# Kernel optimization log

Measured on AMD Instinct MI355X. Metric: run time of the kernel, lower is better.

The kernel has to match this reference:

```python
import jax, jax.numpy as jnp
import numpy as np

EPS = 1e-12

def _l2norm(v):
    return v / (jnp.linalg.norm(v) + EPS)

def _spectral_norm_weight(W, u):
    # torch spectral_norm with n_power_iterations=1: v = norm(W^T u); u' = norm(W v);
    # sigma = u'^T W v with u', v detached; returns W / sigma.
    v = jax.lax.stop_gradient(_l2norm(W.T @ u))
    u2 = jax.lax.stop_gradient(_l2norm(W @ v))
    sigma = u2 @ (W @ v)
    return W / sigma

def setup_inputs() -> dict:
    key = jax.random.key(0)
    ks = jax.random.split(key, 8)
    C, H, W = 64, 96, 96
    Cfg = C // 8
    g = 1e-2  # small weight scale (module uses orthogonal init with tiny gain)
    return {
        "x":  jax.random.normal(ks[0], (1, C, H, W), jnp.float32),
        "Wf": jax.random.normal(ks[1], (Cfg, C), jnp.float32) * g,
        "bf": jnp.zeros((Cfg,), jnp.float32),
        "Wg": jax.random.normal(ks[2], (Cfg, C), jnp.float32) * g,
        "bg": jnp.zeros((Cfg,), jnp.float32),
        "Wh": jax.random.normal(ks[3], (C, C), jnp.float32) * g,
        "bh": jnp.zeros((C,), jnp.float32),
        "gamma": jax.random.normal(ks[4], (1,), jnp.float32),
        "uf": jax.random.normal(ks[5], (Cfg,), jnp.float32),
        "ug": jax.random.normal(ks[6], (Cfg,), jnp.float32),
        "uh": jax.random.normal(ks[7], (C,), jnp.float32),
    }

def reference(x, Wf, bf, Wg, bg, Wh, bh, gamma, uf, ug, uh):
    B, C, H, Wd = x.shape
    N = H * Wd
    xf = x.reshape(B, C, N)  # 1x1 convs act per-pixel -> matmul over channel dim
    Wf_sn = _spectral_norm_weight(Wf, uf)
    Wg_sn = _spectral_norm_weight(Wg, ug)
    Wh_sn = _spectral_norm_weight(Wh, uh)
    f_flat = jnp.einsum('oc,bcn->bon', Wf_sn, xf) + bf[:, None]  # [B,Cfg,N]
    g_flat = jnp.einsum('oc,bcn->bon', Wg_sn, xf) + bg[:, None]  # [B,Cfg,N]
    h_flat = jnp.einsum('oc,bcn->bon', Wh_sn, xf) + bh[:, None]  # [B,C,N]
    # s[b,n,m] = sum_k g[b,k,n] * f[b,k,m]  (g^T f)
    s = jnp.einsum('bkn,bkm->bnm', g_flat, f_flat)  # [B,N,N]
    beta = jax.nn.softmax(s, axis=1)                # softmax over dim=1 (g axis)
    o = jnp.einsum('bcn,bnm->bcm', h_flat, beta)    # [B,C,N]
    o = o.reshape(B, C, H, Wd)
    return gamma * o + x
```

## Files before the change

kernel.cpp:

```cpp
#include <hip/hip_runtime.h>
#include <hip/hip_bf16.h>

#define NPIX 9216
#define MTILES (NPIX / 16)

typedef __attribute__((ext_vector_type(4))) float f32x4;
typedef __attribute__((ext_vector_type(16))) float f32x16;
typedef __attribute__((ext_vector_type(8))) short bf16x8;
typedef __attribute__((ext_vector_type(2))) unsigned int u32x2;

__device__ __forceinline__ void gload_lds16(const void* g, void* l) {
  __builtin_amdgcn_global_load_lds(
      (const __attribute__((address_space(1))) unsigned int*)g,
      (__attribute__((address_space(3))) unsigned int*)l, 16, 0, 0);
}
__device__ __forceinline__ void gload_lds4(const void* g, void* l) {
  __builtin_amdgcn_global_load_lds(
      (const __attribute__((address_space(1))) unsigned int*)g,
      (__attribute__((address_space(3))) unsigned int*)l, 4, 0, 0);
}
#define LDS_OFF(p) ((unsigned)(unsigned long long)(const __attribute__((address_space(3))) char*)(const char*)(p))

__global__ __launch_bounds__(256) void fgh_kernel(
    const float* __restrict__ x,
    const float* __restrict__ Wf, const float* __restrict__ bfv,
    const float* __restrict__ Wg, const float* __restrict__ bgv,
    const float* __restrict__ Wh, const float* __restrict__ bhv,
    const float* __restrict__ uf, const float* __restrict__ ug,
    const float* __restrict__ uh,
    ushort* __restrict__ Qp, ushort* __restrict__ Kp, ushort* __restrict__ Vt2) {
  __shared__ float vsh3[3][64];
  __shared__ float is_s[3];
  const int tid = threadIdx.x;
  const int wv = tid >> 6, t = tid & 63;
  if (wv < 3) {
    const float* W = (wv == 0) ? Wf : (wv == 1) ? Wg : Wh;
    const float* u = (wv == 0) ? uf : (wv == 1) ? ug : uh;
    const int O = (wv == 2) ? 64 : 8;
    float v = 0.f;
    for (int o = 0; o < O; ++o) v += W[o * 64 + t] * u[o];
    float s = v * v;
    for (int off = 32; off; off >>= 1) s += __shfl_xor(s, off);
    vsh3[wv][t] = v / (sqrtf(s) + 1e-12f);
    float wvv = 0.f;
    if (t < O) { for (int c = 0; c < 64; ++c) wvv += W[t * 64 + c] * vsh3[wv][c]; }
    float s2 = (t < O) ? wvv * wvv : 0.f;
    for (int off = 32; off; off >>= 1) s2 += __shfl_xor(s2, off);
    const float nw = sqrtf(s2);
    if (t == 0) is_s[wv] = (nw + 1e-12f) / s2;
  }
  __syncthreads();

  const float LOG2E = 1.44269504f;
  const int px = tid & 63;
  const int rw = __builtin_amdgcn_readfirstlane(tid >> 6);
  const int r0 = blockIdx.y * 16 + rw * 4;
  const int p  = blockIdx.x * 64 + px;

  float xv[64];
  #pragma unroll
  for (int c = 0; c < 64; ++c) xv[c] = x[c * NPIX + p];

  const float* W0;
  float scl;
  if (r0 < 8)       { W0 = Wf + r0 * 64;        scl = is_s[0]; }
  else if (r0 < 16) { W0 = Wg + (r0 - 8) * 64;  scl = is_s[1]; }
  else              { W0 = Wh + (r0 - 16) * 64; scl = is_s[2]; }

  float acc[4] = {0.f, 0.f, 0.f, 0.f};
  #pragma unroll
  for (int c = 0; c < 64; ++c) {
    const float xc = xv[c];
    acc[0] += W0[c]       * xc;
    acc[1] += W0[64 + c]  * xc;
    acc[2] += W0[128 + c] * xc;
    acc[3] += W0[192 + c] * xc;
  }

  const int tile = p >> 5, nn = p & 31;
  const int kbase = tile * 512 + nn * 8;
  const int vfix = (nn >> 4) * 512 + ((nn >> 2) & 1) * 256
                 + (nn & 3) + 4 * ((nn >> 3) & 1);
  #pragma unroll
  for (int j = 0; j < 4; ++j) {
    const int r = r0 + j;
    if (r < 8) {
      const float val = (acc[j] * scl + bfv[r]) * LOG2E;
      const __hip_bfloat16 h = __float2bfloat16(val);
      Qp[p * 16 + r] = *(const ushort*)&h;
    } else if (r < 16) {
      const int rk = r - 8;
      const float val = acc[j] * scl + bgv[rk];
      const __hip_bfloat16 h = __float2bfloat16(val);
      Kp[kbase + rk] = *(const ushort*)&h;
    } else {
      const int rv = r - 16;
      const float val = acc[j] * scl + bhv[rv];
      const __hip_bfloat16 hv = __float2bfloat16(val);
      const int vidx = tile * 2048 + (rv >> 5) * 1024 + vfix + (rv & 31) * 8;
      Vt2[vidx] = *(const ushort*)&hv;
    }
  }
}

template <int S>
__global__ __launch_bounds__(256) void attn_kernel(
    const ushort* __restrict__ Qp, const ushort* __restrict__ Kp,
    const ushort* __restrict__ Vt2,
    ushort* __restrict__ Om,
    float* __restrict__ Sm) {
  constexpr int NSEG = NPIX / S;
  constexpr int NT = NSEG / 32;
  __shared__ ushort Vs[4][2048];
  __shared__ ushort Ks[4][512];
  const int tid  = threadIdx.x;
  const int w    = tid >> 6;
  const int l    = tid & 63;
  const int cc   = l & 31;
  const int h    = l >> 5;
  const int spl  = blockIdx.y;
  const int mrow = blockIdx.x * 128 + w * 32 + cc;

  bf16x8 qh = *(const bf16x8*)(Qp + mrow * 16);
  const bf16x8 zero8 = {0, 0, 0, 0, 0, 0, 0, 0};
  if (l >= 32) qh = zero8;
  asm volatile("" : "+v"(qh));

  const int n0 = spl * NSEG;
  const char* vsrc = (const char*)Vt2 + ((size_t)(n0 >> 5)) * 4096 + w * 1024 + l * 16;
  const char* ksrc = (const char*)Kp + ((size_t)(n0 >> 5)) * 1024 + w * 256 + l * 4;

  #define STAGE(t_) do {                                                  \
    const int b_ = (t_) & 3;                                              \
    gload_lds16(vsrc + (size_t)(t_) * 4096, (char*)&Vs[b_][0] + w * 1024);\
    gload_lds4 (ksrc + (size_t)(t_) * 1024, (char*)&Ks[b_][0] + w * 256); \
  } while (0)

  STAGE(0);
  STAGE(1);

  const unsigned ks_base = LDS_OFF(&Ks[0][0]);
  const unsigned vs_base = LDS_OFF(&Vs[0][0]);

  float ls = 0.f;
  const f32x16 zero16 = {0.f,0.f,0.f,0.f,0.f,0.f,0.f,0.f,
                         0.f,0.f,0.f,0.f,0.f,0.f,0.f,0.f};
  f32x16 accL = zero16, accH = zero16;

  for (int t = 0; t < NT; ++t) {
    const int b = t & 3;
    if (t + 2 < NT) {
      STAGE(t + 2);
      asm volatile("s_waitcnt vmcnt(4)" ::: "memory");
    } else if (t + 1 < NT) {
      asm volatile("s_waitcnt vmcnt(2)" ::: "memory");
    } else {
      asm volatile("s_waitcnt vmcnt(0)" ::: "memory");
    }
    __builtin_amdgcn_s_barrier();

    const unsigned kaddr = ks_base + b * 1024 + cc * 16;
    const unsigned vaddr = vs_base + b * 4096 + l * 16;
    bf16x8 kf, v00, v01, v10, v11;
    asm volatile("ds_read_b128 %0, %1"            : "=v"(kf)  : "v"(kaddr));
    asm volatile("ds_read_b128 %0, %1"            : "=v"(v00) : "v"(vaddr));
    asm volatile("ds_read_b128 %0, %1 offset:1024": "=v"(v01) : "v"(vaddr));
    asm volatile("ds_read_b128 %0, %1 offset:2048": "=v"(v10) : "v"(vaddr));
    asm volatile("ds_read_b128 %0, %1 offset:3072": "=v"(v11) : "v"(vaddr));
    asm volatile("s_waitcnt lgkmcnt(4)" ::: "memory");
    __builtin_amdgcn_sched_barrier(0);

    f32x16 s = zero16;
    s = __builtin_amdgcn_mfma_f32_32x32x16_bf16(kf, qh, s, 0, 0, 0);

    float pj[16];
    #pragma unroll
    for (int r = 0; r < 16; ++r) pj[r] = exp2f(s[r] - 16.f);
    float lsum = 0.f;
    #pragma unroll
    for (int r = 0; r < 16; ++r) lsum += pj[r];
    ls += lsum;

    union { unsigned int u[4]; bf16x8 v; } pa0, pa1;
    #pragma unroll
    for (int jj = 0; jj < 4; ++jj) {
      unsigned int ra, rb;
      asm("v_cvt_pk_bf16_f32 %0, %1, %2" : "=v"(ra) : "v"(pj[2 * jj]), "v"(pj[2 * jj + 1]));
      asm("v_cvt_pk_bf16_f32 %0, %1, %2" : "=v"(rb) : "v"(pj[8 + 2 * jj]), "v"(pj[9 + 2 * jj]));
      pa0.u[jj] = ra;
      pa1.u[jj] = rb;
    }

    asm volatile("s_waitcnt lgkmcnt(0)" ::: "memory");
    __builtin_amdgcn_sched_barrier(0);
    accL = __builtin_amdgcn_mfma_f32_32x32x16_bf16(pa0.v, v00, accL, 0, 0, 0);
    accL = __builtin_amdgcn_mfma_f32_32x32x16_bf16(pa1.v, v01, accL, 0, 0, 0);
    accH = __builtin_amdgcn_mfma_f32_32x32x16_bf16(pa0.v, v10, accH, 0, 0, 0);
    accH = __builtin_amdgcn_mfma_f32_32x32x16_bf16(pa1.v, v11, accH, 0, 0, 0);
  }
  #undef STAGE

  ls += __shfl_xor(ls, 32);

  const size_t mt0 = (size_t)blockIdx.x * 8 + w * 2;
  ushort* Ob0 = Om + (mt0 * S + spl) * 1024;
  ushort* Ob1 = Om + ((mt0 + 1) * S + spl) * 1024;
  float*  Sb0 = Sm + (mt0 * S + spl) * 32;
  float*  Sb1 = Sm + ((mt0 + 1) * S + spl) * 32;
  #pragma unroll
  for (int ch = 0; ch < 2; ++ch) {
    const f32x16 a = (ch == 0) ? accL : accH;
    #pragma unroll
    for (int r = 0; r < 16; r += 2) {
      unsigned int pk;
      asm("v_cvt_pk_bf16_f32 %0, %1, %2" : "=v"(pk) : "v"(a[r]), "v"(a[r + 1]));
      const int m16 = (r & 3) + 8 * ((r >> 2) & 1) + 4 * h;
      ushort* Ob = (r < 8) ? Ob0 : Ob1;
      *(unsigned int*)(Ob + (ch * 32 + cc) * 16 + m16) = pk;
    }
  }
  if (l < 32) {
    float* SbX = (l < 16) ? Sb0 : Sb1;
    SbX[16 + (l & 15)] = ls;
  }
}

template <int S>
__global__ __launch_bounds__(256) void combine_kernel(
    const ushort* __restrict__ Om, const float* __restrict__ Sm,
    const float* __restrict__ x, const float* __restrict__ gammap,
    float* __restrict__ out) {
  const int mt = blockIdx.x >> 2;
  const int m0 = mt * 16;
  const int e  = (blockIdx.x & 3) * 256 + threadIdx.x;
  const float gamma = gammap[0];
  const float* Sb = Sm + (size_t)mt * S * 32;
  const ushort* Ob = Om + (size_t)mt * S * 1024;
  const int m = e & 15, c = e >> 4;
  float L = 0.f, val = 0.f;
  #pragma unroll
  for (int s = 0; s < S; ++s) {
    L += Sb[s * 32 + 16 + m];
    union { unsigned int i; float f; } cv;
    cv.i = ((unsigned int)Ob[s * 1024 + e]) << 16;
    val += cv.f;
  }
  const int idx = c * NPIX + m0 + m;
  out[idx] = gamma * (val / L) + x[idx];
}

extern "C" void kernel_launch(void* const* d_in, const int* in_sizes, int n_in,
                              void* d_out, int out_size, void* d_ws, size_t ws_size,
                              hipStream_t stream) {
  const float* x     = (const float*)d_in[0];
  const float* Wf    = (const float*)d_in[1];
  const float* bf    = (const float*)d_in[2];
  const float* Wg    = (const float*)d_in[3];
  const float* bg    = (const float*)d_in[4];
  const float* Wh    = (const float*)d_in[5];
  const float* bh    = (const float*)d_in[6];
  const float* gamma = (const float*)d_in[7];
  const float* uf    = (const float*)d_in[8];
  const float* ug    = (const float*)d_in[9];
  const float* uh    = (const float*)d_in[10];
  float* out = (float*)d_out;

  char* ws = (char*)d_ws;
  ushort* Qp  = (ushort*)(ws + 256);
  ushort* Kp  = (ushort*)(ws + 256 + NPIX * 16 * 2);
  ushort* Vt2 = (ushort*)(ws + 256 + 2 * NPIX * 16 * 2);
  const size_t off = 256 + (size_t)2 * NPIX * 16 * 2 + (size_t)NPIX * 64 * 2;
  ushort* Om = (ushort*)(ws + off);
  const size_t need16 = off + (size_t)MTILES * 16 * 1024 * 2 + (size_t)MTILES * 16 * 32 * 4;

  fgh_kernel<<<dim3(NPIX / 64, 5), 256, 0, stream>>>(x, Wf, bf, Wg, bg, Wh, bh,
                                                     uf, ug, uh, Qp, Kp, Vt2);
  if (ws_size >= need16) {
    float* Sm = (float*)(ws + off + (size_t)MTILES * 16 * 1024 * 2);
    attn_kernel<16><<<dim3(NPIX / 128, 16), 256, 0, stream>>>(Qp, Kp, Vt2, Om, Sm);
    combine_kernel<16><<<MTILES * 4, 256, 0, stream>>>(Om, Sm, x, gamma, out);
  } else {
    float* Sm = (float*)(ws + off + (size_t)MTILES * 8 * 1024 * 2);
    attn_kernel<8><<<dim3(NPIX / 128, 8), 256, 0, stream>>>(Qp, Kp, Vt2, Om, Sm);
    combine_kernel<8><<<MTILES * 4, 256, 0, stream>>>(Om, Sm, x, gamma, out);
  }
}
```

Before: 72.02 us.

## Process two key tiles per iteration with deeper LDS ring and setprio

The attention loop now handles two 32-key tiles per iteration. The LDS ring grows from 4 to 8 stages with a prefetch distance of 4 tiles, and the second tile's LDS reads are issued while the first tile's exp and PV MFMAs run. It also raises wave priority around the compute section. The aim is to halve barrier count and hide LDS and global latency behind compute. In exchange it doubles LDS usage, which may lower occupancy, and increases register pressure. Correctness assumes NT is even.

```diff
diff --git a/kernel.cpp b/kernel.cpp
--- a/kernel.cpp
+++ b/kernel.cpp
@@ -111,8 +111,8 @@
     float* __restrict__ Sm) {
   constexpr int NSEG = NPIX / S;
   constexpr int NT = NSEG / 32;
-  __shared__ ushort Vs[4][2048];
-  __shared__ ushort Ks[4][512];
+  __shared__ ushort Vs[8][2048];
+  __shared__ ushort Ks[8][512];
   const int tid  = threadIdx.x;
   const int w    = tid >> 6;
   const int l    = tid & 63;
@@ -131,13 +131,12 @@
   const char* ksrc = (const char*)Kp + ((size_t)(n0 >> 5)) * 1024 + w * 256 + l * 4;
 
   #define STAGE(t_) do {                                                  \
-    const int b_ = (t_) & 3;                                              \
+    const int b_ = (t_) & 7;                                              \
     gload_lds16(vsrc + (size_t)(t_) * 4096, (char*)&Vs[b_][0] + w * 1024);\
     gload_lds4 (ksrc + (size_t)(t_) * 1024, (char*)&Ks[b_][0] + w * 256); \
   } while (0)
 
-  STAGE(0);
-  STAGE(1);
+  STAGE(0); STAGE(1); STAGE(2); STAGE(3);
 
   const unsigned ks_base = LDS_OFF(&Ks[0][0]);
   const unsigned vs_base = LDS_OFF(&Vs[0][0]);
@@ -147,56 +146,93 @@
                          0.f,0.f,0.f,0.f,0.f,0.f,0.f,0.f};
   f32x16 accL = zero16, accH = zero16;
 
-  for (int t = 0; t < NT; ++t) {
-    const int b = t & 3;
-    if (t + 2 < NT) {
-      STAGE(t + 2);
+  for (int t = 0; t < NT; t += 2) {
+    if (t + 4 < NT) {
+      STAGE(t + 4); STAGE(t + 5);
+      asm volatile("s_waitcnt vmcnt(8)" ::: "memory");
+    } else if (t + 2 < NT) {
       asm volatile("s_waitcnt vmcnt(4)" ::: "memory");
-    } else if (t + 1 < NT) {
-      asm volatile("s_waitcnt vmcnt(2)" ::: "memory");
     } else {
       asm volatile("s_waitcnt vmcnt(0)" ::: "memory");
     }
     __builtin_amdgcn_s_barrier();
 
-    const unsigned kaddr = ks_base + b * 1024 + cc * 16;
-    const unsigned vaddr = vs_base + b * 4096 + l * 16;
-    bf16x8 kf, v00, v01, v10, v11;
-    asm volatile("ds_read_b128 %0, %1"            : "=v"(kf)  : "v"(kaddr));
-    asm volatile("ds_read_b128 %0, %1"            : "=v"(v00) : "v"(vaddr));
-    asm volatile("ds_read_b128 %0, %1 offset:1024": "=v"(v01) : "v"(vaddr));
-    asm volatile("ds_read_b128 %0, %1 offset:2048": "=v"(v10) : "v"(vaddr));
-    asm volatile("ds_read_b128 %0, %1 offset:3072": "=v"(v11) : "v"(vaddr));
+    const int bA = t & 7, bB = (t + 1) & 7;
+    const unsigned kaddrA = ks_base + bA * 1024 + cc * 16;
+    const unsigned vaddrA = vs_base + bA * 4096 + l * 16;
+    const unsigned kaddrB = ks_base + bB * 1024 + cc * 16;
+    const unsigned vaddrB = vs_base + bB * 4096 + l * 16;
+
+    bf16x8 kfA, vA0, vA1, vA2, vA3, kfB, vB0, vB1, vB2, vB3;
+    asm volatile("ds_read_b128 %0, %1"            : "=v"(kfA) : "v"(kaddrA));
+    asm volatile("ds_read_b128 %0, %1"            : "=v"(vA0) : "v"(vaddrA));
+    asm volatile("ds_read_b128 %0, %1 offset:1024": "=v"(vA1) : "v"(vaddrA));
+    asm volatile("ds_read_b128 %0, %1 offset:2048": "=v"(vA2) : "v"(vaddrA));
+    asm volatile("ds_read_b128 %0, %1 offset:3072": "=v"(vA3) : "v"(vaddrA));
     asm volatile("s_waitcnt lgkmcnt(4)" ::: "memory");
     __builtin_amdgcn_sched_barrier(0);
-
-    f32x16 s = zero16;
-    s = __builtin_amdgcn_mfma_f32_32x32x16_bf16(kf, qh, s, 0, 0, 0);
-
-    float pj[16];
-    #pragma unroll
-    for (int r = 0; r < 16; ++r) pj[r] = exp2f(s[r] - 16.f);
-    float lsum = 0.f;
-    #pragma unroll
-    for (int r = 0; r < 16; ++r) lsum += pj[r];
-    ls += lsum;
-
+    __builtin_amdgcn_s_setprio(1);
+
+    f32x16 sA = zero16;
+    sA = __builtin_amdgcn_mfma_f32_32x32x16_bf16(kfA, qh, sA, 0, 0, 0);
+
+    asm volatile("ds_read_b128 %0, %1"            : "=v"(kfB) : "v"(kaddrB));
+    asm volatile("ds_read_b128 %0, %1"            : "=v"(vB0) : "v"(vaddrB));
+    asm volatile("ds_read_b128 %0, %1 offset:1024": "=v"(vB1) : "v"(vaddrB));
+    asm volatile("ds_read_b128 %0, %1 offset:2048": "=v"(vB2) : "v"(vaddrB));
+    asm volatile("ds_read_b128 %0, %1 offset:3072": "=v"(vB3) : "v"(vaddrB));
+
+    float pjA[16];
+    #pragma unroll
+    for (int r = 0; r < 16; ++r) pjA[r] = exp2f(sA[r] - 16.f);
+    float lsumA = 0.f;
+    #pragma unroll
+    for (int r = 0; r < 16; ++r) lsumA += pjA[r];
+    ls += lsumA;
     union { unsigned int u[4]; bf16x8 v; } pa0, pa1;
     #pragma unroll
     for (int jj = 0; jj < 4; ++jj) {
       unsigned int ra, rb;
-      asm("v_cvt_pk_bf16_f32 %0, %1, %2" : "=v"(ra) : "v"(pj[2 * jj]), "v"(pj[2 * jj + 1]));
-      asm("v_cvt_pk_bf16_f32 %0, %1, %2" : "=v"(rb) : "v"(pj[8 + 2 * jj]), "v"(pj[9 + 2 * jj]));
+      asm("v_cvt_pk_bf16_f32 %0, %1, %2" : "=v"(ra) : "v"(pjA[2 * jj]), "v"(pjA[2 * jj + 1]));
+      asm("v_cvt_pk_bf16_f32 %0, %1, %2" : "=v"(rb) : "v"(pjA[8 + 2 * jj]), "v"(pjA[9 + 2 * jj]));
       pa0.u[jj] = ra;
       pa1.u[jj] = rb;
     }
-
+    asm volatile("s_waitcnt lgkmcnt(5)" ::: "memory");
+    __builtin_amdgcn_sched_barrier(0);
+    accL = __builtin_amdgcn_mfma_f32_32x32x16_bf16(pa0.v, vA0, accL, 0, 0, 0);
+    accL = __builtin_amdgcn_mfma_f32_32x32x16_bf16(pa1.v, vA1, accL, 0, 0, 0);
+    accH = __builtin_amdgcn_mfma_f32_32x32x16_bf16(pa0.v, vA2, accH, 0, 0, 0);
+    accH = __builtin_amdgcn_mfma_f32_32x32x16_bf16(pa1.v, vA3, accH, 0, 0, 0);
+
+    asm volatile("s_waitcnt lgkmcnt(4)" ::: "memory");
+    __builtin_amdgcn_sched_barrier(0);
+    f32x16 sB = zero16;
+    sB = __builtin_amdgcn_mfma_f32_32x32x16_bf16(kfB, qh, sB, 0, 0, 0);
+
+    float pjB[16];
+    #pragma unroll
+    for (int r = 0; r < 16; ++r) pjB[r] = exp2f(sB[r] - 16.f);
+    float lsumB = 0.f;
+    #pragma unroll
+    for (int r = 0; r < 16; ++r) lsumB += pjB[r];
+    ls += lsumB;
+    union { unsigned int u[4]; bf16x8 v; } pb0, pb1;
+    #pragma unroll
+    for (int jj = 0; jj < 4; ++jj) {
+      unsigned int ra, rb;
+      asm("v_cvt_pk_bf16_f32 %0, %1, %2" : "=v"(ra) : "v"(pjB[2 * jj]), "v"(pjB[2 * jj + 1]));
+      asm("v_cvt_pk_bf16_f32 %0, %1, %2" : "=v"(rb) : "v"(pjB[8 + 2 * jj]), "v"(pjB[9 + 2 * jj]));
+      pb0.u[jj] = ra;
+      pb1.u[jj] = rb;
+    }
     asm volatile("s_waitcnt lgkmcnt(0)" ::: "memory");
     __builtin_amdgcn_sched_barrier(0);
-    accL = __builtin_amdgcn_mfma_f32_32x32x16_bf16(pa0.v, v00, accL, 0, 0, 0);
-    accL = __builtin_amdgcn_mfma_f32_32x32x16_bf16(pa1.v, v01, accL, 0, 0, 0);
-    accH = __builtin_amdgcn_mfma_f32_32x32x16_bf16(pa0.v, v10, accH, 0, 0, 0);
-    accH = __builtin_amdgcn_mfma_f32_32x32x16_bf16(pa1.v, v11, accH, 0, 0, 0);
+    accL = __builtin_amdgcn_mfma_f32_32x32x16_bf16(pb0.v, vB0, accL, 0, 0, 0);
+    accL = __builtin_amdgcn_mfma_f32_32x32x16_bf16(pb1.v, vB1, accL, 0, 0, 0);
+    accH = __builtin_amdgcn_mfma_f32_32x32x16_bf16(pb0.v, vB2, accH, 0, 0, 0);
+    accH = __builtin_amdgcn_mfma_f32_32x32x16_bf16(pb1.v, vB3, accH, 0, 0, 0);
+    __builtin_amdgcn_s_setprio(0);
   }
   #undef STAGE
 
```

Result: no change. 72.03 us (+0.0%).

## Fuse split-softmax combine into attention kernel via per-tile atomic counters

Applied to the files above, without the earlier changes.

Removes the separate combine kernel launch on the main path. Each attention wave increments an atomic counter per 16-row tile after writing its partial output and row sums, and the last of the 16 splits performs the combine for that tile. Counters are zeroed in the projection kernel. This saves a launch and a kernel boundary, but the combine now runs serially inside a single wave with a strided loop, and it adds threadfence and atomic traffic.

```diff
diff --git a/kernel.cpp b/kernel.cpp
--- a/kernel.cpp
+++ b/kernel.cpp
@@ -28,10 +28,12 @@
     const float* __restrict__ Wh, const float* __restrict__ bhv,
     const float* __restrict__ uf, const float* __restrict__ ug,
     const float* __restrict__ uh,
-    ushort* __restrict__ Qp, ushort* __restrict__ Kp, ushort* __restrict__ Vt2) {
+    ushort* __restrict__ Qp, ushort* __restrict__ Kp, ushort* __restrict__ Vt2,
+    unsigned* __restrict__ cnt) {
   __shared__ float vsh3[3][64];
   __shared__ float is_s[3];
   const int tid = threadIdx.x;
+  if (blockIdx.y == 0 && tid < 4) cnt[blockIdx.x * 4 + tid] = 0;
   const int wv = tid >> 6, t = tid & 63;
   if (wv < 3) {
     const float* W = (wv == 0) ? Wf : (wv == 1) ? Wg : Wh;
@@ -103,12 +105,35 @@
   }
 }
 
-template <int S>
+__device__ __forceinline__ void wave_combine(
+    int mt, int l, const ushort* __restrict__ Om, const float* __restrict__ Sm,
+    const float* __restrict__ x, float gamma, float* __restrict__ out) {
+  const float* Sb = Sm + (size_t)mt * 16 * 32;
+  const ushort* Ob = Om + (size_t)mt * 16 * 1024;
+  for (int e = l; e < 1024; e += 64) {
+    const int m = e & 15, c = e >> 4;
+    float L = 0.f, val = 0.f;
+    #pragma unroll
+    for (int s = 0; s < 16; ++s) {
+      L += Sb[s * 32 + 16 + m];
+      union { unsigned int i; float f; } cv;
+      cv.i = ((unsigned int)Ob[s * 1024 + e]) << 16;
+      val += cv.f;
+    }
+    const int idx = c * NPIX + mt * 16 + m;
+    out[idx] = gamma * (val / L) + x[idx];
+  }
+}
+
 __global__ __launch_bounds__(256) void attn_kernel(
     const ushort* __restrict__ Qp, const ushort* __restrict__ Kp,
     const ushort* __restrict__ Vt2,
     ushort* __restrict__ Om,
-    float* __restrict__ Sm) {
+    float* __restrict__ Sm,
+    unsigned* __restrict__ cnt,
+    const float* __restrict__ x, const float* __restrict__ gammap,
+    float* __restrict__ out) {
+  constexpr int S = 16;
   constexpr int NSEG = NPIX / S;
   constexpr int NT = NSEG / 32;
   __shared__ ushort Vs[4][2048];
@@ -202,11 +227,11 @@
 
   ls += __shfl_xor(ls, 32);
 
-  const size_t mt0 = (size_t)blockIdx.x * 8 + w * 2;
-  ushort* Ob0 = Om + (mt0 * S + spl) * 1024;
-  ushort* Ob1 = Om + ((mt0 + 1) * S + spl) * 1024;
-  float*  Sb0 = Sm + (mt0 * S + spl) * 32;
-  float*  Sb1 = Sm + ((mt0 + 1) * S + spl) * 32;
+  const int mt0 = blockIdx.x * 8 + w * 2;
+  ushort* Ob0 = Om + ((size_t)mt0 * S + spl) * 1024;
+  ushort* Ob1 = Om + ((size_t)(mt0 + 1) * S + spl) * 1024;
+  float*  Sb0 = Sm + ((size_t)mt0 * S + spl) * 32;
+  float*  Sb1 = Sm + ((size_t)(mt0 + 1) * S + spl) * 32;
   #pragma unroll
   for (int ch = 0; ch < 2; ++ch) {
     const f32x16 a = (ch == 0) ? accL : accH;
@@ -222,6 +247,24 @@
   if (l < 32) {
     float* SbX = (l < 16) ? Sb0 : Sb1;
     SbX[16 + (l & 15)] = ls;
+  }
+
+  __threadfence();
+  unsigned old0 = 0, old1 = 0;
+  if (l == 0) {
+    old0 = atomicAdd(&cnt[mt0], 1u);
+    old1 = atomicAdd(&cnt[mt0 + 1], 1u);
+  }
+  old0 = __shfl(old0, 0);
+  old1 = __shfl(old1, 0);
+  const float gamma = gammap[0];
+  if (old0 == S - 1) {
+    __threadfence();
+    wave_combine(mt0, l, Om, Sm, x, gamma, out);
+  }
+  if (old1 == S - 1) {
+    __threadfence();
+    wave_combine(mt0 + 1, l, Om, Sm, x, gamma, out);
   }
 }
 
@@ -247,6 +290,116 @@
   }
   const int idx = c * NPIX + m0 + m;
   out[idx] = gamma * (val / L) + x[idx];
+}
+
+__global__ __launch_bounds__(256) void attn_kernel8(
+    const ushort* __restrict__ Qp, const ushort* __restrict__ Kp,
+    const ushort* __restrict__ Vt2,
+    ushort* __restrict__ Om, float* __restrict__ Sm) {
+  constexpr int S = 8;
+  constexpr int NSEG = NPIX / S;
+  constexpr int NT = NSEG / 32;
+  __shared__ ushort Vs[4][2048];
+  __shared__ ushort Ks[4][512];
+  const int tid  = threadIdx.x;
+  const int w    = tid >> 6;
+  const int l    = tid & 63;
+  const int cc   = l & 31;
+  const int h    = l >> 5;
+  const int spl  = blockIdx.y;
+  const int mrow = blockIdx.x * 128 + w * 32 + cc;
+
+  bf16x8 qh = *(const bf16x8*)(Qp + mrow * 16);
+  const bf16x8 zero8 = {0, 0, 0, 0, 0, 0, 0, 0};
+  if (l >= 32) qh = zero8;
+  asm volatile("" : "+v"(qh));
+
+  const int n0 = spl * NSEG;
+  const char* vsrc = (const char*)Vt2 + ((size_t)(n0 >> 5)) * 4096 + w * 1024 + l * 16;
+  const char* ksrc = (const char*)Kp + ((size_t)(n0 >> 5)) * 1024 + w * 256 + l * 4;
+
+  #define STAGE(t_) do {                                                  \
+    const int b_ = (t_) & 3;                                              \
+    gload_lds16(vsrc + (size_t)(t_) * 4096, (char*)&Vs[b_][0] + w * 1024);\
+    gload_lds4 (ksrc + (size_t)(t_) * 1024, (char*)&Ks[b_][0] + w * 256); \
+  } while (0)
+  STAGE(0);
+  STAGE(1);
+  const unsigned ks_base = LDS_OFF(&Ks[0][0]);
+  const unsigned vs_base = LDS_OFF(&Vs[0][0]);
+  float ls = 0.f;
+  const f32x16 zero16 = {0.f,0.f,0.f,0.f,0.f,0.f,0.f,0.f,
+                         0.f,0.f,0.f,0.f,0.f,0.f,0.f,0.f};
+  f32x16 accL = zero16, accH = zero16;
+  for (int t = 0; t < NT; ++t) {
+    const int b = t & 3;
+    if (t + 2 < NT) {
+      STAGE(t + 2);
+      asm volatile("s_waitcnt vmcnt(4)" ::: "memory");
+    } else if (t + 1 < NT) {
+      asm volatile("s_waitcnt vmcnt(2)" ::: "memory");
+    } else {
+      asm volatile("s_waitcnt vmcnt(0)" ::: "memory");
+    }
+    __builtin_amdgcn_s_barrier();
+    const unsigned kaddr = ks_base + b * 1024 + cc * 16;
+    const unsigned vaddr = vs_base + b * 4096 + l * 16;
+    bf16x8 kf, v00, v01, v10, v11;
+    asm volatile("ds_read_b128 %0, %1"            : "=v"(kf)  : "v"(kaddr));
+    asm volatile("ds_read_b128 %0, %1"            : "=v"(v00) : "v"(vaddr));
+    asm volatile("ds_read_b128 %0, %1 offset:1024": "=v"(v01) : "v"(vaddr));
+    asm volatile("ds_read_b128 %0, %1 offset:2048": "=v"(v10) : "v"(vaddr));
+    asm volatile("ds_read_b128 %0, %1 offset:3072": "=v"(v11) : "v"(vaddr));
+    asm volatile("s_waitcnt lgkmcnt(4)" ::: "memory");
+    __builtin_amdgcn_sched_barrier(0);
+    f32x16 s = zero16;
+    s = __builtin_amdgcn_mfma_f32_32x32x16_bf16(kf, qh, s, 0, 0, 0);
+    float pj[16];
+    #pragma unroll
+    for (int r = 0; r < 16; ++r) pj[r] = exp2f(s[r] - 16.f);
+    float lsum = 0.f;
+    #pragma unroll
+    for (int r = 0; r < 16; ++r) lsum += pj[r];
+    ls += lsum;
+    union { unsigned int u[4]; bf16x8 v; } pa0, pa1;
+    #pragma unroll
+    for (int jj = 0; jj < 4; ++jj) {
+      unsigned int ra, rb;
+      asm("v_cvt_pk_bf16_f32 %0, %1, %2" : "=v"(ra) : "v"(pj[2 * jj]), "v"(pj[2 * jj + 1]));
+      asm("v_cvt_pk_bf16_f32 %0, %1, %2" : "=v"(rb) : "v"(pj[8 + 2 * jj]), "v"(pj[9 + 2 * jj]));
+      pa0.u[jj] = ra;
+      pa1.u[jj] = rb;
+    }
+    asm volatile("s_waitcnt lgkmcnt(0)" ::: "memory");
+    __builtin_amdgcn_sched_barrier(0);
+    accL = __builtin_amdgcn_mfma_f32_32x32x16_bf16(pa0.v, v00, accL, 0, 0, 0);
+    accL = __builtin_amdgcn_mfma_f32_32x32x16_bf16(pa1.v, v01, accL, 0, 0, 0);
+    accH = __builtin_amdgcn_mfma_f32_32x32x16_bf16(pa0.v, v10, accH, 0, 0, 0);
+    accH = __builtin_amdgcn_mfma_f32_32x32x16_bf16(pa1.v, v11, accH, 0, 0, 0);
+  }
+  #undef STAGE
+  ls += __shfl_xor(ls, 32);
+  const size_t mt0 = (size_t)blockIdx.x * 8 + w * 2;
+  ushort* Ob0 = Om + (mt0 * S + spl) * 1024;
+  ushort* Ob1 = Om + ((mt0 + 1) * S + spl) * 1024;
+  float*  Sb0 = Sm + (mt0 * S + spl) * 32;
+  float*  Sb1 = Sm + ((mt0 + 1) * S + spl) * 32;
+  #pragma unroll
+  for (int ch = 0; ch < 2; ++ch) {
+    const f32x16 a = (ch == 0) ? accL : accH;
+    #pragma unroll
+    for (int r = 0; r < 16; r += 2) {
+      unsigned int pk;
+      asm("v_cvt_pk_bf16_f32 %0, %1, %2" : "=v"(pk) : "v"(a[r]), "v"(a[r + 1]));
+      const int m16 = (r & 3) + 8 * ((r >> 2) & 1) + 4 * h;
+      ushort* Ob = (r < 8) ? Ob0 : Ob1;
+      *(unsigned int*)(Ob + (ch * 32 + cc) * 16 + m16) = pk;
+    }
+  }
+  if (l < 32) {
+    float* SbX = (l < 16) ? Sb0 : Sb1;
+    SbX[16 + (l & 15)] = ls;
+  }
 }
 
 extern "C" void kernel_launch(void* const* d_in, const int* in_sizes, int n_in,
@@ -271,17 +424,24 @@
   ushort* Vt2 = (ushort*)(ws + 256 + 2 * NPIX * 16 * 2);
   const size_t off = 256 + (size_t)2 * NPIX * 16 * 2 + (size_t)NPIX * 64 * 2;
   ushort* Om = (ushort*)(ws + off);
-  const size_t need16 = off + (size_t)MTILES * 16 * 1024 * 2 + (size_t)MTILES * 16 * 32 * 4;
-
-  fgh_kernel<<<dim3(NPIX / 64, 5), 256, 0, stream>>>(x, Wf, bf, Wg, bg, Wh, bh,
-                                                     uf, ug, uh, Qp, Kp, Vt2);
+  const size_t omSz16 = (size_t)MTILES * 16 * 1024 * 2;
+  const size_t smSz16 = (size_t)MTILES * 16 * 32 * 4;
+  const size_t need16 = off + omSz16 + smSz16 + MTILES * 4;
+
   if (ws_size >= need16) {
-    float* Sm = (float*)(ws + off + (size_t)MTILES * 16 * 1024 * 2);
-    attn_kernel<16><<<dim3(NPIX / 128, 16), 256, 0, stream>>>(Qp, Kp, Vt2, Om, Sm);
-    combine_kernel<16><<<MTILES * 4, 256, 0, stream>>>(Om, Sm, x, gamma, out);
+    float*    Sm  = (float*)(ws + off + omSz16);
+    unsigned* cnt = (unsigned*)(ws + off + omSz16 + smSz16);
+    fgh_kernel<<<dim3(NPIX / 64, 5), 256, 0, stream>>>(x, Wf, bf, Wg, bg, Wh, bh,
+                                                       uf, ug, uh, Qp, Kp, Vt2, cnt);
+    attn_kernel<<<dim3(NPIX / 128, 16), 256, 0, stream>>>(Qp, Kp, Vt2, Om, Sm,
+                                                          cnt, x, gamma, out);
   } else {
-    float* Sm = (float*)(ws + off + (size_t)MTILES * 8 * 1024 * 2);
-    attn_kernel<8><<<dim3(NPIX / 128, 8), 256, 0, stream>>>(Qp, Kp, Vt2, Om, Sm);
+    float*    Sm  = (float*)(ws + off + (size_t)MTILES * 8 * 1024 * 2);
+    unsigned* cnt = (unsigned*)(ws + off + (size_t)MTILES * 8 * 1024 * 2 +
+                                (size_t)MTILES * 8 * 32 * 4);
+    fgh_kernel<<<dim3(NPIX / 64, 5), 256, 0, stream>>>(x, Wf, bf, Wg, bg, Wh, bh,
+                                                       uf, ug, uh, Qp, Kp, Vt2, cnt);
+    attn_kernel8<<<dim3(NPIX / 128, 8), 256, 0, stream>>>(Qp, Kp, Vt2, Om, Sm);
     combine_kernel<8><<<MTILES * 4, 256, 0, stream>>>(Om, Sm, x, gamma, out);
   }
 }
```

Result: slower. 211.0 us (+192.9%).
